# Kernel tuning notes

Measured on AMD Instinct MI355X. Metric: run time of the kernel, lower is better.

Reference implementation:

```python
import jax, jax.numpy as jnp
import numpy as np

N_NODES = 10000
N_EDGES = 320000
IN_DIM = 256
OUT_DIM = 256
N_REL = 16


def setup_inputs() -> dict:
    key = jax.random.key(0)
    k_x, k_src, k_dst, k_et, k_wr, k_w0 = jax.random.split(key, 6)
    x = jax.random.normal(k_x, (N_NODES, IN_DIM), dtype=jnp.float32)
    src = jax.random.randint(k_src, (N_EDGES,), 0, N_NODES)
    dst = jax.random.randint(k_dst, (N_EDGES,), 0, N_NODES)
    edge_index = jnp.stack([src, dst], axis=0)  # [2, E]
    edge_type = jax.random.randint(k_et, (N_EDGES,), 0, N_REL)
    # Xavier-uniform-ish init for weights
    lim_r = float(np.sqrt(6.0 / (IN_DIM + OUT_DIM)))
    W_r = jax.random.uniform(k_wr, (N_REL, IN_DIM, OUT_DIM), minval=-lim_r, maxval=lim_r, dtype=jnp.float32)
    W0_w = jax.random.uniform(k_w0, (OUT_DIM, IN_DIM), minval=-lim_r, maxval=lim_r, dtype=jnp.float32)
    W0_b = jnp.zeros((OUT_DIM,), dtype=jnp.float32)
    return {
        "x": x,
        "W_r": W_r,
        "W0_w": W0_w,
        "W0_b": W0_b,
        "edge_index": edge_index,
        "edge_type": edge_type,
        "num_nodes_local": N_NODES,
    }


def reference(x, W_r, W0_w, W0_b, edge_index, edge_type, num_nodes_local):
    N = num_nodes_local
    R = W_r.shape[0]
    src = edge_index[0]
    dst = edge_index[1]
    # Per-(relation, dst-node) in-degree, clamped at 1 (matches deg_r.clamp_min(1))
    deg = jnp.zeros((R, N), dtype=x.dtype).at[edge_type, dst].add(1.0)
    deg = jnp.maximum(deg, 1.0)  # [R, N]
    # Transform all nodes under every relation weight: grouped GEMM [R, N, out]
    h_all = jnp.einsum('nd,rdo->rno', x, W_r)
    # Gather per-edge message and normalize by relation-specific dst degree
    msg = h_all[edge_type, src] / deg[edge_type, dst][:, None]  # [E, out]
    # Scatter-add messages to destination nodes
    agg = jax.ops.segment_sum(msg, dst, num_segments=N)  # [N, out]
    # Self-loop transform W_0(x)
    return agg + x @ W0_w.T + W0_b
```

## Files before the change

kernel.cpp:

```cpp
#include <hip/hip_runtime.h>

typedef __bf16 bf16x8 __attribute__((ext_vector_type(8)));
typedef float f32x4 __attribute__((ext_vector_type(4)));

static __device__ __forceinline__ unsigned short f2bf(float f) {
    union { float f; unsigned int u; } v; v.f = f;
    unsigned int r = v.u + 0x7fffu + ((v.u >> 16) & 1u);
    return (unsigned short)(r >> 16);
}
static __device__ __forceinline__ float blo(unsigned int u) {
    union { unsigned int u; float f; } v; v.u = u << 16; return v.f;
}
static __device__ __forceinline__ float bhi(unsigned int u) {
    union { unsigned int u; float f; } v; v.u = u & 0xffff0000u; return v.f;
}
static __device__ __forceinline__ unsigned int pack2(float a, float b) {
    return (unsigned int)f2bf(a) | ((unsigned int)f2bf(b) << 16);
}

__global__ void zero_kernel(int* __restrict__ p, int n) {
    int i = blockIdx.x * blockDim.x + threadIdx.x;
    int n4 = n >> 2;
    if (i < n4) reinterpret_cast<int4*>(p)[i] = make_int4(0, 0, 0, 0);
    if (i < (n & 3)) p[(n4 << 2) + i] = 0;
}

__global__ __launch_bounds__(256) void prep_kernel(
    const int* __restrict__ dst, const int* __restrict__ et,
    int* __restrict__ deg, int* __restrict__ eoff,
    const float* __restrict__ x, unsigned short* __restrict__ s,
    const float* __restrict__ Wr, const float* __restrict__ W0w,
    unsigned short* __restrict__ Wt2,
    int E, int N, int R, int nh, int nx)
{
    __shared__ float t[64][65];
    const int bid = blockIdx.x, tid = threadIdx.x;
    const int K = (R + 1) * 256;
    if (bid < nh) {
        int i = bid * 256 + tid;
        if (i < E) eoff[i] = atomicAdd(&deg[et[i] * N + dst[i]], 1);
    } else if (bid < nh + nx) {
        int id = (bid - nh) * 256 + tid;
        int n = id >> 6, c4 = id & 63;
        if (n < N) {
            float4 v = *reinterpret_cast<const float4*>(&x[((size_t)n << 8) + (c4 << 2)]);
            ushort4 h;
            h.x = f2bf(v.x); h.y = f2bf(v.y); h.z = f2bf(v.z); h.w = f2bf(v.w);
            *reinterpret_cast<ushort4*>(&s[(size_t)n * K + (K - 256) + (c4 << 2)]) = h;
        }
    } else {
        int tb = bid - nh - nx;
        int sl = tb >> 4, d0 = ((tb >> 2) & 3) * 64, o0 = (tb & 3) * 64;
        if (sl < R) {
            #pragma unroll
            for (int j = 0; j < 16; ++j) {
                int idx = j * 256 + tid;
                int dr = idx >> 6, oc = idx & 63;
                t[dr][oc] = Wr[((size_t)sl * 256 + d0 + dr) * 256 + o0 + oc];
            }
            __syncthreads();
            #pragma unroll
            for (int j = 0; j < 4; ++j) {
                int idx = j * 256 + tid;
                int orow = idx >> 4, dc4 = (idx & 15) << 2;
                ushort4 h;
                h.x = f2bf(t[dc4 + 0][orow]); h.y = f2bf(t[dc4 + 1][orow]);
                h.z = f2bf(t[dc4 + 2][orow]); h.w = f2bf(t[dc4 + 3][orow]);
                *reinterpret_cast<ushort4*>(&Wt2[(size_t)(o0 + orow) * K + sl * 256 + d0 + dc4]) = h;
            }
        } else {
            #pragma unroll
            for (int j = 0; j < 4; ++j) {
                int idx = j * 256 + tid;
                int orow = idx >> 4, dc4 = (idx & 15) << 2;
                float4 v = *reinterpret_cast<const float4*>(&W0w[(size_t)(o0 + orow) * 256 + d0 + dc4]);
                ushort4 h;
                h.x = f2bf(v.x); h.y = f2bf(v.y); h.z = f2bf(v.z); h.w = f2bf(v.w);
                *reinterpret_cast<ushort4*>(&Wt2[(size_t)(o0 + orow) * K + sl * 256 + d0 + dc4]) = h;
            }
        }
    }
}

__global__ void scan1_kernel(const int* __restrict__ deg, int* __restrict__ local,
                             int* __restrict__ bsum, int B) {
    __shared__ int tmp[256];
    int t = threadIdx.x, g = blockIdx.x * 256 + t;
    int v = (g < B) ? deg[g] : 0;
    tmp[t] = v; __syncthreads();
    for (int o = 1; o < 256; o <<= 1) {
        int u = (t >= o) ? tmp[t - o] : 0;
        __syncthreads();
        tmp[t] += u;
        __syncthreads();
    }
    if (g < B) local[g] = tmp[t] - v;
    if (t == 255) bsum[blockIdx.x] = tmp[t];
}

__global__ void scan2_kernel(const int* __restrict__ bsum, int* __restrict__ base, int nc) {
    __shared__ int tmp[1024];
    int t = threadIdx.x;
    int v = (t < nc) ? bsum[t] : 0;
    tmp[t] = v; __syncthreads();
    for (int o = 1; o < 1024; o <<= 1) {
        int u = (t >= o) ? tmp[t - o] : 0;
        __syncthreads();
        tmp[t] += u;
        __syncthreads();
    }
    if (t < nc) base[t] = tmp[t] - v;
}

__global__ void scatter_ids_kernel(const int* __restrict__ src, const int* __restrict__ dst,
                                   const int* __restrict__ et, const int* __restrict__ local,
                                   const int* __restrict__ base, const int* __restrict__ eoff,
                                   int* __restrict__ srcs, int E, int N) {
    int i = blockIdx.x * blockDim.x + threadIdx.x;
    if (i < E) {
        int b = et[i] * N + dst[i];
        srcs[local[b] + base[b >> 8] + eoff[i]] = src[i];
    }
}

__global__ __launch_bounds__(256) void reduce_kernel(
    const int* __restrict__ srcs, const int* __restrict__ deg,
    const int* __restrict__ local, const int* __restrict__ base,
    unsigned short* __restrict__ s, int N, int R)
{
    const int K = (R + 1) * 256;
    const int r = blockIdx.y;
    const int dn = blockIdx.x * 8 + (threadIdx.x >> 5);
    if (dn >= N) return;
    const int lane = threadIdx.x & 31;
    const int bin = r * N + dn;
    const int cnt = deg[bin];
    const int st  = local[bin] + base[bin >> 8];

    float a0 = 0.f, a1 = 0.f, a2 = 0.f, a3 = 0.f;
    float a4 = 0.f, a5 = 0.f, a6 = 0.f, a7 = 0.f;
    for (int c0 = 0; c0 < cnt; c0 += 32) {
        int sv = 0;
        if (c0 + lane < cnt) sv = srcs[st + c0 + lane];
        int m = cnt - c0; if (m > 32) m = 32;
        for (int i = 0; i < m; ++i) {
            int sn = __shfl(sv, i, 32);
            const uint4 v = *reinterpret_cast<const uint4*>(
                &s[(size_t)sn * K + (K - 256) + (lane << 3)]);
            a0 += blo(v.x); a1 += bhi(v.x);
            a2 += blo(v.y); a3 += bhi(v.y);
            a4 += blo(v.z); a5 += bhi(v.z);
            a6 += blo(v.w); a7 += bhi(v.w);
        }
    }
    if (cnt > 0) {
        float sc = 1.0f / (float)cnt;
        a0 *= sc; a1 *= sc; a2 *= sc; a3 *= sc;
        a4 *= sc; a5 *= sc; a6 *= sc; a7 *= sc;
    }
    uint4 o;
    o.x = pack2(a0, a1); o.y = pack2(a2, a3);
    o.z = pack2(a4, a5); o.w = pack2(a6, a7);
    *reinterpret_cast<uint4*>(&s[(size_t)dn * K + (r << 8) + (lane << 3)]) = o;
}

__global__ __launch_bounds__(256) void gemm_kernel(
    const unsigned short* __restrict__ S, const unsigned short* __restrict__ Wt2,
    const float* __restrict__ bias, float* __restrict__ dest,
    int M, int K, int ksteps, int addbias)
{
    __shared__ __align__(16) unsigned short ldsA[2][8192];
    __shared__ __align__(16) unsigned short ldsB[8192];
    const int tid = threadIdx.x;
    const int lane = tid & 63, w = tid >> 6;
    const int wm = w & 1, wn = w >> 1;

    const int nM = gridDim.y;
    const int nwg = 2 * nM * gridDim.z;
    int L = blockIdx.x + 2 * (blockIdx.y + nM * blockIdx.z);
    if ((nwg & 7) == 0) { int q = nwg >> 3; L = (L & 7) * q + (L >> 3); }
    const int z = L / (2 * nM);
    const int rem = L - z * (2 * nM);
    const int m0 = (rem >> 1) * 128, n0 = (rem & 1) * 128;
    const int kstart = z * ksteps * 64;
    const size_t rowb = (size_t)K * 2;

    f32x4 acc[4][4] = {};

    const int flat_base = w * 4 * 64 + lane;

#define STAGE_A(buf, kstep)                                                               \
    {                                                                                     \
        const int kb = (kstart + (kstep) * 64) * 2;                                       \
        _Pragma("unroll")                                                                 \
        for (int i = 0; i < 4; ++i) {                                                     \
            int flat = flat_base + i * 64;                                                \
            int row = flat >> 3, seg = flat & 7;                                          \
            int gr = m0 + row; gr = gr < M ? gr : M - 1;                                  \
            const char* gp = (const char*)S + (size_t)gr * rowb + kb                      \
                             + ((seg * 16) ^ ((row & 7) << 4));                           \
            unsigned short* lp = &ldsA[buf][(w * 4 + i) * 512];                           \
            __builtin_amdgcn_global_load_lds(                                             \
                (const __attribute__((address_space(1))) void*)gp,                        \
                (__attribute__((address_space(3))) void*)lp, 16, 0, 0);                   \
        }                                                                                 \
    }

#define STAGE_B(kstep)                                                                    \
    {                                                                                     \
        const int kb = (kstart + (kstep) * 64) * 2;                                       \
        _Pragma("unroll")                                                                 \
        for (int i = 0; i < 4; ++i) {                                                     \
            int flat = flat_base + i * 64;                                                \
            int row = flat >> 3, seg = flat & 7;                                          \
            const char* gp = (const char*)Wt2 + (size_t)(n0 + row) * rowb + kb            \
                             + ((seg * 16) ^ ((row & 7) << 4));                           \
            unsigned short* lp = &ldsB[(w * 4 + i) * 512];                                \
            __builtin_amdgcn_global_load_lds(                                             \
                (const __attribute__((address_space(1))) void*)gp,                        \
                (__attribute__((address_space(3))) void*)lp, 16, 0, 0);                   \
        }                                                                                 \
    }

#define COMPUTE(buf)                                                                      \
    {                                                                                     \
        _Pragma("unroll")                                                                 \
        for (int kk = 0; kk < 2; ++kk) {                                                  \
            bf16x8 af[4], bfr[4];                                                         \
            _Pragma("unroll")                                                             \
            for (int m = 0; m < 4; ++m) {                                                 \
                int row = wm * 64 + m * 16 + (lane & 15);                                 \
                int colb = (kk * 64 + ((lane >> 4) << 4)) ^ ((row & 7) << 4);             \
                af[m] = *reinterpret_cast<const bf16x8*>(                                 \
                    (const char*)&ldsA[buf][0] + row * 128 + colb);                       \
            }                                                                             \
            _Pragma("unroll")                                                             \
            for (int n = 0; n < 4; ++n) {                                                 \
                int row = wn * 64 + n * 16 + (lane & 15);                                 \
                int colb = (kk * 64 + ((lane >> 4) << 4)) ^ ((row & 7) << 4);             \
                bfr[n] = *reinterpret_cast<const bf16x8*>(                                \
                    (const char*)&ldsB[0] + row * 128 + colb);                            \
            }                                                                             \
            __builtin_amdgcn_s_setprio(1);                                                \
            _Pragma("unroll")                                                             \
            for (int m = 0; m < 4; ++m)                                                   \
                _Pragma("unroll")                                                         \
                for (int n = 0; n < 4; ++n)                                               \
                    acc[m][n] = __builtin_amdgcn_mfma_f32_16x16x32_bf16(                  \
                        af[m], bfr[n], acc[m][n], 0, 0, 0);                               \
            __builtin_amdgcn_s_setprio(0);                                                \
        }                                                                                 \
    }

    STAGE_A(0, 0)
    STAGE_B(0)
    STAGE_A(1, 1)
    asm volatile("s_waitcnt vmcnt(4)" ::: "memory");
    __builtin_amdgcn_s_barrier();

    for (int t = 0; t < ksteps; ++t) {
        COMPUTE(t & 1)
        asm volatile("s_waitcnt lgkmcnt(0)" ::: "memory");
        __builtin_amdgcn_sched_barrier(0);
        __builtin_amdgcn_s_barrier();
        if (t + 1 < ksteps) {
            STAGE_B(t + 1)
            if (t + 2 < ksteps) {
                STAGE_A(t & 1, t + 2)
                asm volatile("s_waitcnt vmcnt(4)" ::: "memory");
            } else {
                asm volatile("s_waitcnt vmcnt(0)" ::: "memory");
            }
            __builtin_amdgcn_s_barrier();
        }
    }
#undef STAGE_A
#undef STAGE_B
#undef COMPUTE

    float* dst = dest + (size_t)z * M * 256;
    if (addbias) dst = dest;
    const int rbase = m0 + wm * 64 + ((lane >> 4) << 2);
    const int cbase = n0 + wn * 64 + (lane & 15);
    #pragma unroll
    for (int n = 0; n < 4; ++n) {
        int c = cbase + n * 16;
        float bv = addbias ? bias[c] : 0.0f;
        #pragma unroll
        for (int m = 0; m < 4; ++m) {
            #pragma unroll
            for (int j = 0; j < 4; ++j) {
                int r = rbase + m * 16 + j;
                if (r < M) dst[(size_t)r * 256 + c] = acc[m][n][j] + bv;
            }
        }
    }
}

__global__ void combine_kernel(const float* __restrict__ pbuf, const float* __restrict__ bias,
                               float* __restrict__ out, int M, int KZ) {
    int id = blockIdx.x * blockDim.x + threadIdx.x;
    if (id >= M * 64) return;
    int n = id >> 6, c4 = id & 63;
    float4 a = *reinterpret_cast<const float4*>(&pbuf[((size_t)n << 8) + (c4 << 2)]);
    for (int kz = 1; kz < KZ; ++kz) {
        float4 b = *reinterpret_cast<const float4*>(&pbuf[(size_t)kz * M * 256 + ((size_t)n << 8) + (c4 << 2)]);
        a.x += b.x; a.y += b.y; a.z += b.z; a.w += b.w;
    }
    const float4 bv = *reinterpret_cast<const float4*>(&bias[c4 << 2]);
    a.x += bv.x; a.y += bv.y; a.z += bv.z; a.w += bv.w;
    *reinterpret_cast<float4*>(&out[((size_t)n << 8) + (c4 << 2)]) = a;
}

extern "C" void kernel_launch(void* const* d_in, const int* in_sizes, int n_in,
                              void* d_out, int out_size, void* d_ws, size_t ws_size,
                              hipStream_t stream) {
    const float* x   = (const float*)d_in[0];
    const float* Wr  = (const float*)d_in[1];
    const float* W0w = (const float*)d_in[2];
    const float* W0b = (const float*)d_in[3];
    const int*   eidx= (const int*)d_in[4];
    const int*   et  = (const int*)d_in[5];
    const int N = in_sizes[0] / 256;
    const int R = in_sizes[1] / 65536;
    const int E = in_sizes[5];
    const int* src = eidx;
    const int* dst = eidx + E;
    float* out = (float*)d_out;

    const int B = R * N;
    const int NC = (B + 255) / 256;
    const int K = (R + 1) * 256;

    const size_t sz_pslice = (size_t)N * 256 * 4;
    const size_t sz_sort = (((size_t)B * 4 + 255) & ~255UL) * 2
                         + (((size_t)E * 4 + 255) & ~255UL) * 2
                         + 2 * 4096;
    const size_t sz_wt2 = (size_t)256 * K * 2;
    const size_t sz_s   = (size_t)N * K * 2;
    int KZ = 1;
    for (int kz = 4; kz >= 1; kz >>= 1) {
        size_t r0 = (kz > 1) ? (size_t)kz * sz_pslice : 0;
        if (sz_sort > r0) r0 = sz_sort;
        size_t need = ((r0 + 255) & ~255UL) + ((sz_wt2 + 255) & ~255UL) + sz_s + 1024;
        if (need <= ws_size || kz == 1) { KZ = kz; break; }
    }

    char* ws = (char*)d_ws;
    size_t off = 0;
    auto alloc = [&](size_t bytes) { void* p = ws + off; off = (off + bytes + 255) & ~(size_t)255; return p; };
    float* pbuf = (float*)ws;
    int* deg    = (int*)alloc((size_t)B * 4);
    int* local  = (int*)alloc((size_t)B * 4);
    int* bsum   = (int*)alloc(4096);
    int* base   = (int*)alloc(4096);
    int* eoff   = (int*)alloc((size_t)E * 4);
    int* srcs   = (int*)alloc((size_t)E * 4);
    size_t region0 = (KZ > 1) ? (size_t)KZ * sz_pslice : 0;
    if (off > region0) region0 = off;
    off = (region0 + 255) & ~(size_t)255;
    unsigned short* Wt2 = (unsigned short*)alloc(sz_wt2);
    unsigned short* s   = (unsigned short*)alloc(sz_s);

    zero_kernel<<<(B / 4 + 255) / 256, 256, 0, stream>>>(deg, B);
    {
        const int nh = (E + 255) / 256;
        const int nx = (N * 64 + 255) / 256;
        const int nwT = (R + 1) * 16;
        prep_kernel<<<nh + nx + nwT, 256, 0, stream>>>(dst, et, deg, eoff, x, s,
                                                       Wr, W0w, Wt2, E, N, R, nh, nx);
    }
    scan1_kernel<<<NC, 256, 0, stream>>>(deg, local, bsum, B);
    scan2_kernel<<<1, 1024, 0, stream>>>(bsum, base, NC);
    scatter_ids_kernel<<<(E + 255) / 256, 256, 0, stream>>>(src, dst, et, local, base, eoff, srcs, E, N);
    {
        dim3 g((N + 7) / 8, R);
        reduce_kernel<<<g, 256, 0, stream>>>(srcs, deg, local, base, s, N, R);
    }
    {
        const int ktot = K / 64;
        const int ksteps = ktot / KZ;
        const int nM = (N + 127) / 128;
        dim3 grid(2, nM, KZ);
        if (KZ == 1) {
            gemm_kernel<<<grid, 256, 0, stream>>>(s, Wt2, W0b, out, N, K, ksteps, 1);
        } else {
            gemm_kernel<<<grid, 256, 0, stream>>>(s, Wt2, W0b, pbuf, N, K, ksteps, 0);
            combine_kernel<<<(N * 64 + 255) / 256, 256, 0, stream>>>(pbuf, W0b, out, N, KZ);
        }
    }
}
```

Baseline: 119.3 us.

## Transform-then-aggregate: GEMM x against all relation weights, then gather per destination

Reverses the order of operations. Previously the code aggregated x per (relation, dst) and ran one big K=(R+1)*256 GEMM. Now it computes h = x·[W_r…, W0] as a wide bf16 GEMM with K=256 and 4352 output columns, sorts edges by dst only (with relation and 1/deg packed per edge), and gathers per dst with the self-loop and bias fused in. This removes the split-K and combine path and the R×N aggregation bins. In exchange it writes and gathers a large bf16 h (N×4352), and the gather reads scattered 512-byte slices of it.

New measurement: 123.5 us. 3.5% more time.

```diff
diff --git a/kernel.cpp b/kernel.cpp
--- a/kernel.cpp
+++ b/kernel.cpp
@@ -13,9 +13,6 @@
 }
 static __device__ __forceinline__ float bhi(unsigned int u) {
     union { unsigned int u; float f; } v; v.u = u & 0xffff0000u; return v.f;
-}
-static __device__ __forceinline__ unsigned int pack2(float a, float b) {
-    return (unsigned int)f2bf(a) | ((unsigned int)f2bf(b) << 16);
 }
 
 __global__ void zero_kernel(int* __restrict__ p, int n) {
@@ -27,18 +24,21 @@
 
 __global__ __launch_bounds__(256) void prep_kernel(
     const int* __restrict__ dst, const int* __restrict__ et,
-    int* __restrict__ deg, int* __restrict__ eoff,
-    const float* __restrict__ x, unsigned short* __restrict__ s,
+    int* __restrict__ deg_rd, int* __restrict__ cnt_d, int* __restrict__ eoff,
+    const float* __restrict__ x, unsigned short* __restrict__ xbf,
     const float* __restrict__ Wr, const float* __restrict__ W0w,
     unsigned short* __restrict__ Wt2,
     int E, int N, int R, int nh, int nx)
 {
     __shared__ float t[64][65];
     const int bid = blockIdx.x, tid = threadIdx.x;
-    const int K = (R + 1) * 256;
     if (bid < nh) {
         int i = bid * 256 + tid;
-        if (i < E) eoff[i] = atomicAdd(&deg[et[i] * N + dst[i]], 1);
+        if (i < E) {
+            int d = dst[i];
+            atomicAdd(&deg_rd[et[i] * N + d], 1);
+            eoff[i] = atomicAdd(&cnt_d[d], 1);
+        }
     } else if (bid < nh + nx) {
         int id = (bid - nh) * 256 + tid;
         int n = id >> 6, c4 = id & 63;
@@ -46,7 +46,7 @@
             float4 v = *reinterpret_cast<const float4*>(&x[((size_t)n << 8) + (c4 << 2)]);
             ushort4 h;
             h.x = f2bf(v.x); h.y = f2bf(v.y); h.z = f2bf(v.z); h.w = f2bf(v.w);
-            *reinterpret_cast<ushort4*>(&s[(size_t)n * K + (K - 256) + (c4 << 2)]) = h;
+            *reinterpret_cast<ushort4*>(&xbf[((size_t)n << 8) + (c4 << 2)]) = h;
         }
     } else {
         int tb = bid - nh - nx;
@@ -66,7 +66,7 @@
                 ushort4 h;
                 h.x = f2bf(t[dc4 + 0][orow]); h.y = f2bf(t[dc4 + 1][orow]);
                 h.z = f2bf(t[dc4 + 2][orow]); h.w = f2bf(t[dc4 + 3][orow]);
-                *reinterpret_cast<ushort4*>(&Wt2[(size_t)(o0 + orow) * K + sl * 256 + d0 + dc4]) = h;
+                *reinterpret_cast<ushort4*>(&Wt2[((size_t)sl * 256 + o0 + orow) * 256 + d0 + dc4]) = h;
             }
         } else {
             #pragma unroll
@@ -76,17 +76,17 @@
                 float4 v = *reinterpret_cast<const float4*>(&W0w[(size_t)(o0 + orow) * 256 + d0 + dc4]);
                 ushort4 h;
                 h.x = f2bf(v.x); h.y = f2bf(v.y); h.z = f2bf(v.z); h.w = f2bf(v.w);
-                *reinterpret_cast<ushort4*>(&Wt2[(size_t)(o0 + orow) * K + sl * 256 + d0 + dc4]) = h;
+                *reinterpret_cast<ushort4*>(&Wt2[((size_t)R * 256 + o0 + orow) * 256 + d0 + dc4]) = h;
             }
         }
     }
 }
 
-__global__ void scan1_kernel(const int* __restrict__ deg, int* __restrict__ local,
+__global__ void scan1_kernel(const int* __restrict__ cnt, int* __restrict__ local,
                              int* __restrict__ bsum, int B) {
     __shared__ int tmp[256];
     int t = threadIdx.x, g = blockIdx.x * 256 + t;
-    int v = (g < B) ? deg[g] : 0;
+    int v = (g < B) ? cnt[g] : 0;
     tmp[t] = v; __syncthreads();
     for (int o = 1; o < 256; o <<= 1) {
         int u = (t >= o) ? tmp[t - o] : 0;
@@ -112,78 +112,31 @@
     if (t < nc) base[t] = tmp[t] - v;
 }
 
-__global__ void scatter_ids_kernel(const int* __restrict__ src, const int* __restrict__ dst,
-                                   const int* __restrict__ et, const int* __restrict__ local,
-                                   const int* __restrict__ base, const int* __restrict__ eoff,
-                                   int* __restrict__ srcs, int E, int N) {
+__global__ void scatter2_kernel(const int* __restrict__ src, const int* __restrict__ dst,
+                                const int* __restrict__ et, const int* __restrict__ local,
+                                const int* __restrict__ base, const int* __restrict__ eoff,
+                                const int* __restrict__ deg_rd, uint2* __restrict__ srcs2,
+                                int E, int N) {
     int i = blockIdx.x * blockDim.x + threadIdx.x;
     if (i < E) {
-        int b = et[i] * N + dst[i];
-        srcs[local[b] + base[b >> 8] + eoff[i]] = src[i];
-    }
-}
-
-__global__ __launch_bounds__(256) void reduce_kernel(
-    const int* __restrict__ srcs, const int* __restrict__ deg,
-    const int* __restrict__ local, const int* __restrict__ base,
-    unsigned short* __restrict__ s, int N, int R)
-{
-    const int K = (R + 1) * 256;
-    const int r = blockIdx.y;
-    const int dn = blockIdx.x * 8 + (threadIdx.x >> 5);
-    if (dn >= N) return;
-    const int lane = threadIdx.x & 31;
-    const int bin = r * N + dn;
-    const int cnt = deg[bin];
-    const int st  = local[bin] + base[bin >> 8];
-
-    float a0 = 0.f, a1 = 0.f, a2 = 0.f, a3 = 0.f;
-    float a4 = 0.f, a5 = 0.f, a6 = 0.f, a7 = 0.f;
-    for (int c0 = 0; c0 < cnt; c0 += 32) {
-        int sv = 0;
-        if (c0 + lane < cnt) sv = srcs[st + c0 + lane];
-        int m = cnt - c0; if (m > 32) m = 32;
-        for (int i = 0; i < m; ++i) {
-            int sn = __shfl(sv, i, 32);
-            const uint4 v = *reinterpret_cast<const uint4*>(
-                &s[(size_t)sn * K + (K - 256) + (lane << 3)]);
-            a0 += blo(v.x); a1 += bhi(v.x);
-            a2 += blo(v.y); a3 += bhi(v.y);
-            a4 += blo(v.z); a5 += bhi(v.z);
-            a6 += blo(v.w); a7 += bhi(v.w);
-        }
-    }
-    if (cnt > 0) {
-        float sc = 1.0f / (float)cnt;
-        a0 *= sc; a1 *= sc; a2 *= sc; a3 *= sc;
-        a4 *= sc; a5 *= sc; a6 *= sc; a7 *= sc;
-    }
-    uint4 o;
-    o.x = pack2(a0, a1); o.y = pack2(a2, a3);
-    o.z = pack2(a4, a5); o.w = pack2(a6, a7);
-    *reinterpret_cast<uint4*>(&s[(size_t)dn * K + (r << 8) + (lane << 3)]) = o;
-}
-
-__global__ __launch_bounds__(256) void gemm_kernel(
+        int d = dst[i], r = et[i];
+        int pos = local[d] + base[d >> 8] + eoff[i];
+        float sc = 1.0f / (float)deg_rd[r * N + d];
+        srcs2[pos] = make_uint2((unsigned)src[i] | ((unsigned)r << 20), __float_as_uint(sc));
+    }
+}
+
+__global__ __launch_bounds__(256) void gemm_h_kernel(
     const unsigned short* __restrict__ S, const unsigned short* __restrict__ Wt2,
-    const float* __restrict__ bias, float* __restrict__ dest,
-    int M, int K, int ksteps, int addbias)
+    unsigned short* __restrict__ h, int M)
 {
     __shared__ __align__(16) unsigned short ldsA[2][8192];
     __shared__ __align__(16) unsigned short ldsB[8192];
     const int tid = threadIdx.x;
     const int lane = tid & 63, w = tid >> 6;
     const int wm = w & 1, wn = w >> 1;
-
-    const int nM = gridDim.y;
-    const int nwg = 2 * nM * gridDim.z;
-    int L = blockIdx.x + 2 * (blockIdx.y + nM * blockIdx.z);
-    if ((nwg & 7) == 0) { int q = nwg >> 3; L = (L & 7) * q + (L >> 3); }
-    const int z = L / (2 * nM);
-    const int rem = L - z * (2 * nM);
-    const int m0 = (rem >> 1) * 128, n0 = (rem & 1) * 128;
-    const int kstart = z * ksteps * 64;
-    const size_t rowb = (size_t)K * 2;
+    const int n0 = blockIdx.x * 128, m0 = blockIdx.y * 128;
+    const int ksteps = 4;
 
     f32x4 acc[4][4] = {};
 
@@ -191,13 +144,13 @@
 
 #define STAGE_A(buf, kstep)                                                               \
     {                                                                                     \
-        const int kb = (kstart + (kstep) * 64) * 2;                                       \
+        const int kb = (kstep) * 128;                                                     \
         _Pragma("unroll")                                                                 \
         for (int i = 0; i < 4; ++i) {                                                     \
             int flat = flat_base + i * 64;                                                \
             int row = flat >> 3, seg = flat & 7;                                          \
             int gr = m0 + row; gr = gr < M ? gr : M - 1;                                  \
-            const char* gp = (const char*)S + (size_t)gr * rowb + kb                      \
+            const char* gp = (const char*)S + (size_t)gr * 512 + kb                       \
                              + ((seg * 16) ^ ((row & 7) << 4));                           \
             unsigned short* lp = &ldsA[buf][(w * 4 + i) * 512];                           \
             __builtin_amdgcn_global_load_lds(                                             \
@@ -208,12 +161,12 @@
 
 #define STAGE_B(kstep)                                                                    \
     {                                                                                     \
-        const int kb = (kstart + (kstep) * 64) * 2;                                       \
+        const int kb = (kstep) * 128;                                                     \
         _Pragma("unroll")                                                                 \
         for (int i = 0; i < 4; ++i) {                                                     \
             int flat = flat_base + i * 64;                                                \
             int row = flat >> 3, seg = flat & 7;                                          \
-            const char* gp = (const char*)Wt2 + (size_t)(n0 + row) * rowb + kb            \
+            const char* gp = (const char*)Wt2 + (size_t)(n0 + row) * 512 + kb             \
                              + ((seg * 16) ^ ((row & 7) << 4));                           \
             unsigned short* lp = &ldsB[(w * 4 + i) * 512];                                \
             __builtin_amdgcn_global_load_lds(                                             \
@@ -278,38 +231,68 @@
 #undef STAGE_B
 #undef COMPUTE
 
-    float* dst = dest + (size_t)z * M * 256;
-    if (addbias) dst = dest;
-    const int rbase = m0 + wm * 64 + ((lane >> 4) << 2);
-    const int cbase = n0 + wn * 64 + (lane & 15);
+    unsigned short* ldsC = &ldsA[0][0];
+    const int lr = wm * 64 + ((lane >> 4) << 2);
+    const int lc = wn * 64 + (lane & 15);
     #pragma unroll
-    for (int n = 0; n < 4; ++n) {
-        int c = cbase + n * 16;
-        float bv = addbias ? bias[c] : 0.0f;
+    for (int n = 0; n < 4; ++n)
         #pragma unroll
-        for (int m = 0; m < 4; ++m) {
+        for (int m = 0; m < 4; ++m)
             #pragma unroll
-            for (int j = 0; j < 4; ++j) {
-                int r = rbase + m * 16 + j;
-                if (r < M) dst[(size_t)r * 256 + c] = acc[m][n][j] + bv;
-            }
-        }
-    }
-}
-
-__global__ void combine_kernel(const float* __restrict__ pbuf, const float* __restrict__ bias,
-                               float* __restrict__ out, int M, int KZ) {
-    int id = blockIdx.x * blockDim.x + threadIdx.x;
-    if (id >= M * 64) return;
-    int n = id >> 6, c4 = id & 63;
-    float4 a = *reinterpret_cast<const float4*>(&pbuf[((size_t)n << 8) + (c4 << 2)]);
-    for (int kz = 1; kz < KZ; ++kz) {
-        float4 b = *reinterpret_cast<const float4*>(&pbuf[(size_t)kz * M * 256 + ((size_t)n << 8) + (c4 << 2)]);
-        a.x += b.x; a.y += b.y; a.z += b.z; a.w += b.w;
-    }
-    const float4 bv = *reinterpret_cast<const float4*>(&bias[c4 << 2]);
-    a.x += bv.x; a.y += bv.y; a.z += bv.z; a.w += bv.w;
-    *reinterpret_cast<float4*>(&out[((size_t)n << 8) + (c4 << 2)]) = a;
+            for (int j = 0; j < 4; ++j)
+                ldsC[(lr + m * 16 + j) * 128 + lc + n * 16] = f2bf(acc[m][n][j]);
+    __syncthreads();
+    #pragma unroll
+    for (int i = 0; i < 8; ++i) {
+        int idx = tid + i * 256;
+        int row = idx >> 4, ch = idx & 15;
+        int gr = m0 + row;
+        if (gr < M)
+            *reinterpret_cast<uint4*>(&h[(size_t)gr * 4352 + n0 + ch * 8]) =
+                *reinterpret_cast<const uint4*>(&ldsC[row * 128 + ch * 8]);
+    }
+}
+
+__global__ __launch_bounds__(256) void reduce2_kernel(
+    const uint2* __restrict__ srcs2, const int* __restrict__ cnt_d,
+    const int* __restrict__ local, const int* __restrict__ base,
+    const unsigned short* __restrict__ h, const float* __restrict__ bias,
+    float* __restrict__ out, int N)
+{
+    const int dn = blockIdx.x * 8 + (threadIdx.x >> 5);
+    if (dn >= N) return;
+    const int lane = threadIdx.x & 31;
+    const int cnt = cnt_d[dn];
+    const int st  = local[dn] + base[dn >> 8];
+
+    float a0 = 0.f, a1 = 0.f, a2 = 0.f, a3 = 0.f;
+    float a4 = 0.f, a5 = 0.f, a6 = 0.f, a7 = 0.f;
+    for (int c0 = 0; c0 < cnt; c0 += 32) {
+        uint2 pv = make_uint2(0u, 0u);
+        if (c0 + lane < cnt) pv = srcs2[st + c0 + lane];
+        int m = cnt - c0; if (m > 32) m = 32;
+        for (int i = 0; i < m; ++i) {
+            unsigned w0 = (unsigned)__shfl((int)pv.x, i, 32);
+            float sc = __int_as_float(__shfl((int)pv.y, i, 32));
+            int sn = (int)(w0 & 0xFFFFFu), r = (int)(w0 >> 20);
+            const uint4 v = *reinterpret_cast<const uint4*>(
+                &h[(size_t)sn * 4352 + r * 256 + (lane << 3)]);
+            a0 += sc * blo(v.x); a1 += sc * bhi(v.x);
+            a2 += sc * blo(v.y); a3 += sc * bhi(v.y);
+            a4 += sc * blo(v.z); a5 += sc * bhi(v.z);
+            a6 += sc * blo(v.w); a7 += sc * bhi(v.w);
+        }
+    }
+    const uint4 sv = *reinterpret_cast<const uint4*>(&h[(size_t)dn * 4352 + 4096 + (lane << 3)]);
+    const float4 b0 = *reinterpret_cast<const float4*>(&bias[(lane << 3)]);
+    const float4 b1 = *reinterpret_cast<const float4*>(&bias[(lane << 3) + 4]);
+    float4 o0, o1;
+    o0.x = a0 + blo(sv.x) + b0.x; o0.y = a1 + bhi(sv.x) + b0.y;
+    o0.z = a2 + blo(sv.y) + b0.z; o0.w = a3 + bhi(sv.y) + b0.w;
+    o1.x = a4 + blo(sv.z) + b1.x; o1.y = a5 + bhi(sv.z) + b1.y;
+    o1.z = a6 + blo(sv.w) + b1.z; o1.w = a7 + bhi(sv.w) + b1.w;
+    *reinterpret_cast<float4*>(&out[(size_t)dn * 256 + (lane << 3)]) = o0;
+    *reinterpret_cast<float4*>(&out[(size_t)dn * 256 + (lane << 3) + 4]) = o1;
 }
 
 extern "C" void kernel_launch(void* const* d_in, const int* in_sizes, int n_in,
@@ -329,64 +312,39 @@
     float* out = (float*)d_out;
 
     const int B = R * N;
-    const int NC = (B + 255) / 256;
+    const int NC2 = (N + 255) / 256;
     const int K = (R + 1) * 256;
-
-    const size_t sz_pslice = (size_t)N * 256 * 4;
-    const size_t sz_sort = (((size_t)B * 4 + 255) & ~255UL) * 2
-                         + (((size_t)E * 4 + 255) & ~255UL) * 2
-                         + 2 * 4096;
-    const size_t sz_wt2 = (size_t)256 * K * 2;
-    const size_t sz_s   = (size_t)N * K * 2;
-    int KZ = 1;
-    for (int kz = 4; kz >= 1; kz >>= 1) {
-        size_t r0 = (kz > 1) ? (size_t)kz * sz_pslice : 0;
-        if (sz_sort > r0) r0 = sz_sort;
-        size_t need = ((r0 + 255) & ~255UL) + ((sz_wt2 + 255) & ~255UL) + sz_s + 1024;
-        if (need <= ws_size || kz == 1) { KZ = kz; break; }
-    }
 
     char* ws = (char*)d_ws;
     size_t off = 0;
     auto alloc = [&](size_t bytes) { void* p = ws + off; off = (off + bytes + 255) & ~(size_t)255; return p; };
-    float* pbuf = (float*)ws;
-    int* deg    = (int*)alloc((size_t)B * 4);
-    int* local  = (int*)alloc((size_t)B * 4);
+    int* deg_rd = (int*)alloc((size_t)B * 4);
+    int* cnt_d  = (int*)alloc((size_t)N * 4);
+    int* local  = (int*)alloc((size_t)N * 4);
     int* bsum   = (int*)alloc(4096);
     int* base   = (int*)alloc(4096);
     int* eoff   = (int*)alloc((size_t)E * 4);
-    int* srcs   = (int*)alloc((size_t)E * 4);
-    size_t region0 = (KZ > 1) ? (size_t)KZ * sz_pslice : 0;
-    if (off > region0) region0 = off;
-    off = (region0 + 255) & ~(size_t)255;
-    unsigned short* Wt2 = (unsigned short*)alloc(sz_wt2);
-    unsigned short* s   = (unsigned short*)alloc(sz_s);
-
-    zero_kernel<<<(B / 4 + 255) / 256, 256, 0, stream>>>(deg, B);
+    uint2* srcs2 = (uint2*)alloc((size_t)E * 8);
+    unsigned short* xbf = (unsigned short*)alloc((size_t)N * 256 * 2);
+    unsigned short* Wt2 = (unsigned short*)alloc((size_t)K * 256 * 2);
+    unsigned short* h   = (unsigned short*)alloc((size_t)N * K * 2);
+    (void)ws_size;
+
+    zero_kernel<<<((B + N) / 4 + 255) / 256, 256, 0, stream>>>(deg_rd, B + N);
     {
         const int nh = (E + 255) / 256;
         const int nx = (N * 64 + 255) / 256;
         const int nwT = (R + 1) * 16;
-        prep_kernel<<<nh + nx + nwT, 256, 0, stream>>>(dst, et, deg, eoff, x, s,
-                                                       Wr, W0w, Wt2, E, N, R, nh, nx);
-    }
-    scan1_kernel<<<NC, 256, 0, stream>>>(deg, local, bsum, B);
-    scan2_kernel<<<1, 1024, 0, stream>>>(bsum, base, NC);
-    scatter_ids_kernel<<<(E + 255) / 256, 256, 0, stream>>>(src, dst, et, local, base, eoff, srcs, E, N);
+        prep_kernel<<<nh + nx + nwT, 256, 0, stream>>>(dst, et, deg_rd, cnt_d, eoff,
+                                                       x, xbf, Wr, W0w, Wt2, E, N, R, nh, nx);
+    }
+    scan1_kernel<<<NC2, 256, 0, stream>>>(cnt_d, local, bsum, N);
+    scan2_kernel<<<1, 1024, 0, stream>>>(bsum, base, NC2);
+    scatter2_kernel<<<(E + 255) / 256, 256, 0, stream>>>(src, dst, et, local, base, eoff,
+                                                         deg_rd, srcs2, E, N);
     {
-        dim3 g((N + 7) / 8, R);
-        reduce_kernel<<<g, 256, 0, stream>>>(srcs, deg, local, base, s, N, R);
-    }
-    {
-        const int ktot = K / 64;
-        const int ksteps = ktot / KZ;
-        const int nM = (N + 127) / 128;
-        dim3 grid(2, nM, KZ);
-        if (KZ == 1) {
-            gemm_kernel<<<grid, 256, 0, stream>>>(s, Wt2, W0b, out, N, K, ksteps, 1);
-        } else {
-            gemm_kernel<<<grid, 256, 0, stream>>>(s, Wt2, W0b, pbuf, N, K, ksteps, 0);
-            combine_kernel<<<(N * 64 + 255) / 256, 256, 0, stream>>>(pbuf, W0b, out, N, KZ);
-        }
-    }
-}
+        dim3 grid(K / 128, (N + 127) / 128);
+        gemm_h_kernel<<<grid, 256, 0, stream>>>(xbf, Wt2, h, N);
+    }
+    reduce2_kernel<<<(N + 7) / 8, 256, 0, stream>>>(srcs2, cnt_d, local, base, h, W0b, out, N);
+}
```
